# Kernel tuning notes

Measured on AMD Instinct MI355X. Metric: run time of the kernel, lower is better.

## Reference

```python
import jax, jax.numpy as jnp
import numpy as np

DIM = 1024
HEADS = 16
HEAD_DIM = DIM // HEADS
MLP_HIDDEN = int(DIM * 0.7)  # 716
EPS = 1e-5


def _ln(x, g, b):
    m = jnp.mean(x, axis=-1, keepdims=True)
    v = jnp.mean(jnp.square(x - m), axis=-1, keepdims=True)
    return (x - m) * jax.lax.rsqrt(v + EPS) * g + b


def setup_inputs() -> dict:
    key = jax.random.key(0)
    ks = jax.random.split(key, 8)
    B, N = 4, 1024
    x = jax.random.normal(ks[0], (B, N, DIM), dtype=jnp.float32)
    s = 0.02
    return {
        "x": x,
        "norm_g": jnp.ones((DIM,), jnp.float32),
        "norm_b": jnp.zeros((DIM,), jnp.float32),
        "W1": jax.random.normal(ks[1], (DIM, 3 * DIM + MLP_HIDDEN), jnp.float32) * s,
        "b1": jnp.zeros((3 * DIM + MLP_HIDDEN,), jnp.float32),
        "qn_g": jnp.ones((HEAD_DIM,), jnp.float32),
        "qn_b": jnp.zeros((HEAD_DIM,), jnp.float32),
        "kn_g": jnp.ones((HEAD_DIM,), jnp.float32),
        "kn_b": jnp.zeros((HEAD_DIM,), jnp.float32),
        "projW": jax.random.normal(ks[2], (DIM, DIM), jnp.float32) * s,
        "projb": jnp.zeros((DIM,), jnp.float32),
        "mlpW": jax.random.normal(ks[3], (MLP_HIDDEN, DIM), jnp.float32) * s,  # mlp_bias=False
        "W2": jax.random.normal(ks[4], (2 * DIM, DIM), jnp.float32) * s,
        "b2": jnp.zeros((DIM,), jnp.float32),
        "ls_g": jnp.full((DIM,), 1e-5, jnp.float32),
    }


def reference(x, norm_g, norm_b, W1, b1, qn_g, qn_b, kn_g, kn_b,
              projW, projb, mlpW, W2, b2, ls_g):
    B, N, C = x.shape
    norm_x = _ln(x, norm_g, norm_b)
    f1 = norm_x @ W1 + b1  # (B, N, 3*dim + mlp_hidden)
    qkv, mlp_hidden = f1[..., :3 * DIM], f1[..., 3 * DIM:]
    # (B, N, 3, H, hd) -> (3, B, H, N, hd)
    qkv = qkv.reshape(B, N, 3, HEADS, HEAD_DIM).transpose(2, 0, 3, 1, 4)
    q, k, v = qkv[0], qkv[1], qkv[2]
    q = _ln(q, qn_g, qn_b)
    k = _ln(k, kn_g, kn_b)
    attn = jnp.einsum('bhnd,bhmd->bhnm', q, k) * (HEAD_DIM ** -0.5)
    attn = jax.nn.softmax(attn, axis=-1)
    xo = jnp.einsum('bhnm,bhmd->bhnd', attn, v)
    xo = xo.transpose(0, 2, 1, 3).reshape(B, N, DIM)
    attn_out = xo @ projW + projb
    mlp_out = jax.nn.gelu(mlp_hidden, approximate=False) @ mlpW  # no bias
    combined = jnp.concatenate([attn_out, mlp_out], axis=-1)
    out = x + (combined @ W2 + b2) * ls_g
    return out
```

## Files before the change

### kernel.cpp

```cpp
#include <hip/hip_runtime.h>
#include <cstdint>
#include <cstddef>

typedef unsigned short u16;
typedef unsigned char u8;
typedef __attribute__((ext_vector_type(8))) u16 u16x8;
typedef __attribute__((ext_vector_type(8))) __bf16 bf16x8;
typedef __attribute__((ext_vector_type(4))) float f32x4;
typedef __attribute__((ext_vector_type(16))) float f32x16;
typedef __attribute__((ext_vector_type(4))) int i32x4;
typedef __attribute__((ext_vector_type(8))) int i32x8;
typedef __attribute__((ext_vector_type(2))) int i32x2;

__device__ __forceinline__ u16 f2bf(float f) {
  unsigned u = __builtin_bit_cast(unsigned, f);
  return (u16)((u + 0x7FFFu + ((u >> 16) & 1u)) >> 16);
}
__device__ __forceinline__ float bf2f(u16 h) {
  return __builtin_bit_cast(float, (unsigned)h << 16);
}
__device__ __forceinline__ u8 f2fp8(float f) {
  return (u8)(__builtin_amdgcn_cvt_pk_fp8_f32(f, 0.f, 0, false) & 0xFF);
}
__device__ __forceinline__ f32x4 mfma16(u16x8 a, u16x8 b, f32x4 c) {
  return __builtin_amdgcn_mfma_f32_16x16x32_bf16(
      __builtin_bit_cast(bf16x8, a), __builtin_bit_cast(bf16x8, b), c, 0, 0, 0);
}
__device__ __forceinline__ f32x16 mfma32(u16x8 a, u16x8 b, f32x16 c) {
  return __builtin_amdgcn_mfma_f32_32x32x16_bf16(
      __builtin_bit_cast(bf16x8, a), __builtin_bit_cast(bf16x8, b), c, 0, 0, 0);
}
__device__ __forceinline__ unsigned cvtpk_bf16(float lo, float hi) {
  unsigned r;
  asm("v_cvt_pk_bf16_f32 %0, %1, %2" : "=v"(r) : "v"(lo), "v"(hi));
  return r;
}
__device__ __forceinline__ void plswap(unsigned& a, unsigned& b) {
  i32x2 r = __builtin_amdgcn_permlane32_swap((int)a, (int)b, false, false);
  a = (unsigned)r[0];
  b = (unsigned)r[1];
}
__device__ __forceinline__ void load_lds16(const void* g, void* l) {
  __builtin_amdgcn_global_load_lds(
      (const __attribute__((address_space(1))) void*)g,
      (__attribute__((address_space(3))) void*)l, 16, 0, 0);
}

__global__ __launch_bounds__(256) void k_pre(
    const float* __restrict__ W1, const float* __restrict__ projW,
    const float* __restrict__ mlpW, const float* __restrict__ W2,
    u8* __restrict__ W1t, u8* __restrict__ pWt, u8* __restrict__ mWt,
    u8* __restrict__ W2t, const float* __restrict__ x,
    const float* __restrict__ g, const float* __restrict__ b,
    u8* __restrict__ nx8) {
  __shared__ float t[32][33];
  __shared__ float red[8];
  const int L = blockIdx.x;
  const int tid = threadIdx.x;
  if (L < 7680) {
    const float* src;
    u8* dst;
    int R, C, dR, dC, bx, by;
    if (L < 3840) {
      src = W1; dst = W1t; R = 1024; C = 3788; dR = 1024; dC = 3840;
      bx = L % 120; by = L / 120;
    } else if (L < 4864) {
      int tq = L - 3840;
      src = projW; dst = pWt; R = 1024; C = 1024; dR = 1024; dC = 1024;
      bx = tq & 31; by = tq >> 5;
    } else if (L < 5632) {
      int tq = L - 4864;
      src = mlpW; dst = mWt; R = 716; C = 1024; dR = 768; dC = 1024;
      bx = tq & 31; by = tq >> 5;
    } else {
      int tq = L - 5632;
      src = W2; dst = W2t; R = 2048; C = 1024; dR = 2048; dC = 1024;
      bx = tq & 31; by = tq >> 5;
    }
    const int n0 = bx * 32, k0 = by * 32;
    const int tx = tid & 31, ty = tid >> 5;
#pragma unroll
    for (int j = 0; j < 4; ++j) {
      int kk = k0 + ty + 8 * j, nn = n0 + tx;
      float v = (kk < R && nn < C) ? src[(size_t)kk * C + nn] : 0.f;
      t[ty + 8 * j][tx] = v;
    }
    __syncthreads();
#pragma unroll
    for (int j = 0; j < 4; ++j) {
      int nn = n0 + ty + 8 * j, kk = k0 + tx;
      if (nn < dC && kk < dR) dst[(size_t)nn * dR + kk] = f2fp8(t[tx][ty + 8 * j]);
    }
  } else {
    const int row = L - 7680;
    float4 v = ((const float4*)(x + (size_t)row * 1024))[tid];
    float s = v.x + v.y + v.z + v.w;
    float ss = v.x * v.x + v.y * v.y + v.z * v.z + v.w * v.w;
#pragma unroll
    for (int off = 1; off < 64; off <<= 1) {
      s += __shfl_xor(s, off);
      ss += __shfl_xor(ss, off);
    }
    const int wid = tid >> 6, lane = tid & 63;
    if (lane == 0) { red[wid] = s; red[4 + wid] = ss; }
    __syncthreads();
    s = red[0] + red[1] + red[2] + red[3];
    ss = red[4] + red[5] + red[6] + red[7];
    const float mean = s * (1.f / 1024.f);
    const float var = ss * (1.f / 1024.f) - mean * mean;
    const float rstd = rsqrtf(var + 1e-5f);
    float4 gv = ((const float4*)g)[tid];
    float4 bv = ((const float4*)b)[tid];
    float y0 = (v.x - mean) * rstd * gv.x + bv.x;
    float y1 = (v.y - mean) * rstd * gv.y + bv.y;
    float y2 = (v.z - mean) * rstd * gv.z + bv.z;
    float y3 = (v.w - mean) * rstd * gv.w + bv.w;
    int pk = __builtin_amdgcn_cvt_pk_fp8_f32(y0, y1, 0, false);
    pk = __builtin_amdgcn_cvt_pk_fp8_f32(y2, y3, pk, true);
    ((int*)(nx8 + (size_t)row * 1024))[tid] = pk;
  }
}

__device__ __forceinline__ void gemm_fp8_core(const u8* __restrict__ A,
                                              const u8* __restrict__ B, int K,
                                              u8* Alds, u8* Blds,
                                              f32x16 (&acc)[2][2], int tid) {
  const int lane = tid & 63, wave = tid >> 6;
  const int h = lane >> 5, r32 = lane & 31;
  const int wrow = (wave >> 1) * 64, wcol = (wave & 1) * 64;
  const int srow0 = tid >> 2, spos = tid & 3;
  const int nk = K >> 6;
#pragma unroll
  for (int p = 0; p < 2; ++p) {
    const int row = p * 64 + srow0;
    const int c = spos ^ ((row >> 1) & 3);
    const size_t go = (size_t)row * K + c * 16;
    load_lds16(A + go, Alds + (p * 256 + tid) * 16);
    load_lds16(B + go, Blds + (p * 256 + tid) * 16);
  }
  __syncthreads();
  for (int kt = 0; kt < nk; ++kt) {
    const int cur = kt & 1;
    const u8* Ac = Alds + cur * 8192;
    const u8* Bc = Blds + cur * 8192;
    if (kt + 1 < nk) {
      u8* An = Alds + (cur ^ 1) * 8192;
      u8* Bn = Blds + (cur ^ 1) * 8192;
#pragma unroll
      for (int p = 0; p < 2; ++p) {
        const int row = p * 64 + srow0;
        const int c = spos ^ ((row >> 1) & 3);
        const size_t go = (size_t)row * K + (size_t)(kt + 1) * 64 + c * 16;
        load_lds16(A + go, An + (p * 256 + tid) * 16);
        load_lds16(B + go, Bn + (p * 256 + tid) * 16);
      }
    }
    i32x8 af[2], bf[2];
#pragma unroll
    for (int t = 0; t < 2; ++t) {
      {
        const int row = wrow + t * 32 + r32;
        const int sw = (row >> 1) & 3;
        i32x4 lo = *(const i32x4*)(Ac + row * 64 + ((2 * h) ^ sw) * 16);
        i32x4 hi = *(const i32x4*)(Ac + row * 64 + ((2 * h + 1) ^ sw) * 16);
        i32x8 a;
        a[0] = lo[0]; a[1] = lo[1]; a[2] = lo[2]; a[3] = lo[3];
        a[4] = hi[0]; a[5] = hi[1]; a[6] = hi[2]; a[7] = hi[3];
        af[t] = a;
      }
      {
        const int row = wcol + t * 32 + r32;
        const int sw = (row >> 1) & 3;
        i32x4 lo = *(const i32x4*)(Bc + row * 64 + ((2 * h) ^ sw) * 16);
        i32x4 hi = *(const i32x4*)(Bc + row * 64 + ((2 * h + 1) ^ sw) * 16);
        i32x8 b8;
        b8[0] = lo[0]; b8[1] = lo[1]; b8[2] = lo[2]; b8[3] = lo[3];
        b8[4] = hi[0]; b8[5] = hi[1]; b8[6] = hi[2]; b8[7] = hi[3];
        bf[t] = b8;
      }
    }
#pragma unroll
    for (int i = 0; i < 2; ++i)
#pragma unroll
      for (int j = 0; j < 2; ++j)
        acc[i][j] = __builtin_amdgcn_mfma_scale_f32_32x32x64_f8f6f4(
            af[i], bf[j], acc[i][j], 0, 0, 0, 0x7F7F7F7F, 0, 0x7F7F7F7F);
    __syncthreads();
  }
}

__device__ __forceinline__ void gemm_fp8_core64(const u8* __restrict__ A,
                                                const u8* __restrict__ B, int K,
                                                u8* Alds, u8* Blds,
                                                f32x16 (&acc)[2], int tid) {
  const int lane = tid & 63, wave = tid >> 6;
  const int h = lane >> 5, r32 = lane & 31;
  const int wrow = (wave >> 1) * 32, wcol = (wave & 1) * 64;
  const int nk = K >> 6;
  const int ra = tid >> 2, posa = tid & 3;
  const int ca = posa ^ ((ra >> 1) & 3);
  load_lds16(A + (size_t)ra * K + ca * 16, Alds + tid * 16);
#pragma unroll
  for (int p = 0; p < 2; ++p) {
    const int s = tid + 256 * p;
    const int r = s >> 2, pos = s & 3;
    const int c = pos ^ ((r >> 1) & 3);
    load_lds16(B + (size_t)r * K + c * 16, Blds + s * 16);
  }
  __syncthreads();
  for (int kt = 0; kt < nk; ++kt) {
    const int cur = kt & 1;
    const u8* Ac = Alds + cur * 4096;
    const u8* Bc = Blds + cur * 8192;
    if (kt + 1 < nk) {
      u8* An = Alds + (cur ^ 1) * 4096;
      u8* Bn = Blds + (cur ^ 1) * 8192;
      const size_t k1 = (size_t)(kt + 1) * 64;
      load_lds16(A + (size_t)ra * K + k1 + ca * 16, An + tid * 16);
#pragma unroll
      for (int p = 0; p < 2; ++p) {
        const int s = tid + 256 * p;
        const int r = s >> 2, pos = s & 3;
        const int c = pos ^ ((r >> 1) & 3);
        load_lds16(B + (size_t)r * K + k1 + c * 16, Bn + s * 16);
      }
    }
    i32x8 af, bf[2];
    {
      const int row = wrow + r32;
      const int sw = (row >> 1) & 3;
      i32x4 lo = *(const i32x4*)(Ac + row * 64 + ((2 * h) ^ sw) * 16);
      i32x4 hi = *(const i32x4*)(Ac + row * 64 + ((2 * h + 1) ^ sw) * 16);
      af[0] = lo[0]; af[1] = lo[1]; af[2] = lo[2]; af[3] = lo[3];
      af[4] = hi[0]; af[5] = hi[1]; af[6] = hi[2]; af[7] = hi[3];
    }
#pragma unroll
    for (int t = 0; t < 2; ++t) {
      const int row = wcol + t * 32 + r32;
      const int sw = (row >> 1) & 3;
      i32x4 lo = *(const i32x4*)(Bc + row * 64 + ((2 * h) ^ sw) * 16);
      i32x4 hi = *(const i32x4*)(Bc + row * 64 + ((2 * h + 1) ^ sw) * 16);
      i32x8 b8;
      b8[0] = lo[0]; b8[1] = lo[1]; b8[2] = lo[2]; b8[3] = lo[3];
      b8[4] = hi[0]; b8[5] = hi[1]; b8[6] = hi[2]; b8[7] = hi[3];
      bf[t] = b8;
    }
#pragma unroll
    for (int j = 0; j < 2; ++j)
      acc[j] = __builtin_amdgcn_mfma_scale_f32_32x32x64_f8f6f4(
          af, bf[j], acc[j], 0, 0, 0, 0x7F7F7F7F, 0, 0x7F7F7F7F);
    __syncthreads();
  }
}

__global__ __launch_bounds__(256) void k_gemm1(const u8* __restrict__ nx8,
                                               const u8* __restrict__ W1t,
                                               u16* __restrict__ f1,
                                               const float* __restrict__ b1) {
  __shared__ __align__(16) u8 Alds[2 * 128 * 64];
  __shared__ __align__(16) u8 Blds[2 * 128 * 64];
  const int tid = threadIdx.x, bm = blockIdx.y, bn = blockIdx.x;
  f32x16 acc[2][2];
#pragma unroll
  for (int i = 0; i < 2; ++i)
#pragma unroll
    for (int j = 0; j < 2; ++j)
#pragma unroll
      for (int r = 0; r < 16; ++r) acc[i][j][r] = 0.f;
  gemm_fp8_core(nx8 + (size_t)bm * 128 * 1024, W1t + (size_t)bn * 128 * 1024, 1024,
                Alds, Blds, acc, tid);
  const int lane = tid & 63, wave = tid >> 6;
  const int h = lane >> 5, r32 = lane & 31;
  const int wrow = (wave >> 1) * 64, wcol = (wave & 1) * 64;
#pragma unroll
  for (int i = 0; i < 2; ++i)
#pragma unroll
    for (int j = 0; j < 2; ++j) {
      const int col = bn * 128 + wcol + j * 32 + r32;
      const float bs = (col < 3788) ? b1[col] : 0.f;
#pragma unroll
      for (int r = 0; r < 16; ++r) {
        const int row = bm * 128 + wrow + i * 32 + 4 * h + (r & 3) + 8 * (r >> 2);
        f1[(size_t)row * 3840 + col] = f2bf(acc[i][j][r] + bs);
      }
    }
}

__global__ __launch_bounds__(256) void k_gemm_pm(
    const u8* __restrict__ xo, const u8* __restrict__ pWt,
    const u8* __restrict__ gel, const u8* __restrict__ mWt,
    u8* __restrict__ comb, const float* __restrict__ projb) {
  __shared__ __align__(16) u8 Alds[2 * 64 * 64];
  __shared__ __align__(16) u8 Blds[2 * 128 * 64];
  const int tid = threadIdx.x, bm = blockIdx.y, bnq = blockIdx.x;
  const u8* A;
  const u8* B;
  int K, colbase;
  const float* bias;
  if (bnq < 8) {
    A = xo + (size_t)bm * 64 * 1024;
    B = pWt + (size_t)bnq * 128 * 1024;
    K = 1024; colbase = bnq * 128; bias = projb;
  } else {
    A = gel + (size_t)bm * 64 * 768;
    B = mWt + (size_t)(bnq - 8) * 128 * 768;
    K = 768; colbase = 1024 + (bnq - 8) * 128; bias = nullptr;
  }
  f32x16 acc[2];
#pragma unroll
  for (int j = 0; j < 2; ++j)
#pragma unroll
    for (int r = 0; r < 16; ++r) acc[j][r] = 0.f;
  gemm_fp8_core64(A, B, K, Alds, Blds, acc, tid);
  const int lane = tid & 63, wave = tid >> 6;
  const int h = lane >> 5, r32 = lane & 31;
  const int wrow = (wave >> 1) * 32, wcol = (wave & 1) * 64;
#pragma unroll
  for (int j = 0; j < 2; ++j) {
    const int col = colbase + wcol + j * 32 + r32;
    const float bs = (bias != nullptr) ? bias[col] : 0.f;
#pragma unroll
    for (int r = 0; r < 16; ++r) {
      const int row = bm * 64 + wrow + 4 * h + (r & 3) + 8 * (r >> 2);
      comb[(size_t)row * 2048 + col] = f2fp8(acc[j][r] + bs);
    }
  }
}

__global__ __launch_bounds__(256) void k_gemm_fin(const u8* __restrict__ comb,
                                                  const u8* __restrict__ W2t,
                                                  float* __restrict__ out,
                                                  const float* __restrict__ b2,
                                                  const float* __restrict__ x,
                                                  const float* __restrict__ lsg) {
  __shared__ __align__(16) u8 Alds[2 * 64 * 64];
  __shared__ __align__(16) u8 Blds[2 * 128 * 64];
  const int tid = threadIdx.x, bm = blockIdx.y, bn = blockIdx.x;
  f32x16 acc[2];
#pragma unroll
  for (int j = 0; j < 2; ++j)
#pragma unroll
    for (int r = 0; r < 16; ++r) acc[j][r] = 0.f;
  gemm_fp8_core64(comb + (size_t)bm * 64 * 2048, W2t + (size_t)bn * 128 * 2048, 2048,
                  Alds, Blds, acc, tid);
  const int lane = tid & 63, wave = tid >> 6;
  const int h = lane >> 5, r32 = lane & 31;
  const int wrow = (wave >> 1) * 32, wcol = (wave & 1) * 64;
#pragma unroll
  for (int j = 0; j < 2; ++j) {
    const int col = bn * 128 + wcol + j * 32 + r32;
    const float bs = b2[col], ls = lsg[col];
#pragma unroll
    for (int r = 0; r < 16; ++r) {
      const int row = bm * 64 + wrow + 4 * h + (r & 3) + 8 * (r >> 2);
      out[(size_t)row * 1024 + col] =
          x[(size_t)row * 1024 + col] + (acc[j][r] + bs) * ls;
    }
  }
}

__global__ __launch_bounds__(256) void k_mid(const u16* __restrict__ f1,
                                             const float* __restrict__ qg,
                                             const float* __restrict__ qbb,
                                             const float* __restrict__ kg,
                                             const float* __restrict__ kbb,
                                             u16* __restrict__ q,
                                             u16* __restrict__ k,
                                             u8* __restrict__ gel,
                                             u16* __restrict__ vtb) {
  __shared__ u16 tt[32][33];
  const int tid = threadIdx.x;
  const int L = blockIdx.x;
  if (L < 4096) {
    const int row = L;
    const int rem = tid >> 3;
    const int which = rem >> 4, h = rem & 15;
    const int e8 = (tid & 7) * 8;
    u16x8 xv = *(const u16x8*)(f1 + (size_t)row * 3840 + which * 1024 + h * 64 + e8);
    float xf[8];
    float s1 = 0.f, s2 = 0.f;
#pragma unroll
    for (int e = 0; e < 8; ++e) {
      xf[e] = bf2f(xv[e]);
      s1 += xf[e];
      s2 += xf[e] * xf[e];
    }
#pragma unroll
    for (int off = 1; off < 8; off <<= 1) {
      s1 += __shfl_xor(s1, off);
      s2 += __shfl_xor(s2, off);
    }
    const float mean = s1 * (1.f / 64.f);
    const float var = s2 * (1.f / 64.f) - mean * mean;
    const float rstd = rsqrtf(var + 1e-5f);
    const float* g = (which == 0) ? qg : kg;
    const float* bb = (which == 0) ? qbb : kbb;
    float4 g0 = ((const float4*)g)[e8 >> 2], g1 = ((const float4*)g)[(e8 >> 2) + 1];
    float4 b0 = ((const float4*)bb)[e8 >> 2], b1 = ((const float4*)bb)[(e8 >> 2) + 1];
    float gv[8] = {g0.x, g0.y, g0.z, g0.w, g1.x, g1.y, g1.z, g1.w};
    float bv[8] = {b0.x, b0.y, b0.z, b0.w, b1.x, b1.y, b1.z, b1.w};
    u16x8 o;
#pragma unroll
    for (int e = 0; e < 8; ++e) o[e] = f2bf((xf[e] - mean) * rstd * gv[e] + bv[e]);
    const int b = row >> 10, n = row & 1023;
    u16* dst = (which == 0) ? q : k;
    *(u16x8*)(dst + ((size_t)(b * 16 + h) * 1024 + n) * 64 + e8) = o;
  } else if (L < 5632) {
    const int id = (L - 4096) * 256 + tid;
    const int row = id / 96, c8 = id - row * 96;
    u16x8 xv = *(const u16x8*)(f1 + (size_t)row * 3840 + 3072 + c8 * 8);
    float rr[8];
#pragma unroll
    for (int e = 0; e < 8; ++e) {
      const int col = c8 * 8 + e;
      rr[e] = 0.f;
      if (col < 716) {
        float xx = bf2f(xv[e]);
        rr[e] = 0.5f * xx * (1.f + erff(xx * 0.70710678118654752f));
      }
    }
    int p0 = __builtin_amdgcn_cvt_pk_fp8_f32(rr[0], rr[1], 0, false);
    p0 = __builtin_amdgcn_cvt_pk_fp8_f32(rr[2], rr[3], p0, true);
    int p1 = __builtin_amdgcn_cvt_pk_fp8_f32(rr[4], rr[5], 0, false);
    p1 = __builtin_amdgcn_cvt_pk_fp8_f32(rr[6], rr[7], p1, true);
    uint2 pk;
    pk.x = (unsigned)p0;
    pk.y = (unsigned)p1;
    *(uint2*)(gel + (size_t)row * 768 + c8 * 8) = pk;
  } else {
    const int t = L - 5632;
    const int xq = t & 1, yq = (t >> 1) & 31, z = t >> 6;
    const int b = z >> 4, h = z & 15;
    const int d0 = xq * 32, n0 = yq * 32;
    const int tx = tid & 31, ty = tid >> 5;
#pragma unroll
    for (int j = 0; j < 4; ++j)
      tt[ty + 8 * j][tx] =
          f1[(size_t)(b * 1024 + n0 + ty + 8 * j) * 3840 + 2048 + h * 64 + d0 + tx];
    __syncthreads();
#pragma unroll
    for (int j = 0; j < 4; ++j)
      vtb[(size_t)z * 65536 + (size_t)(d0 + ty + 8 * j) * 1024 + n0 + tx] =
          tt[tx][ty + 8 * j];
  }
}

__global__ __launch_bounds__(128) void k_flash(const u16* __restrict__ q,
                                               const u16* __restrict__ k,
                                               const u16* __restrict__ vt,
                                               u8* __restrict__ xo) {
  __shared__ __align__(16) u16 Kl[2][64 * 64];
  __shared__ __align__(16) u16 Vl[2][64 * 64];
  const int tid = threadIdx.x, wave = tid >> 6, lane = tid & 63;
  const int l31 = lane & 31, h = lane >> 5;
  const int L = blockIdx.x;
  const int xcd = L & 7, i = L >> 3;
  const int bh = xcd * 8 + (i & 7), qt = i >> 3;
  const int qrow0 = qt * 64 + wave * 32;
  const u16* qb = q + ((size_t)bh * 1024 + qrow0) * 64;
  const u16* kb = k + (size_t)bh * 1024 * 64;
  const u16* vb = vt + (size_t)bh * 64 * 1024;

  u16x8 qf[4];
#pragma unroll
  for (int ds = 0; ds < 4; ++ds)
    qf[ds] = *(const u16x8*)(qb + (size_t)l31 * 64 + ds * 16 + h * 8);

  f32x16 O[2];
#pragma unroll
  for (int d2 = 0; d2 < 2; ++d2)
#pragma unroll
    for (int r = 0; r < 16; ++r) O[d2][r] = 0.f;
  float lacc = 0.f;

  int sr[4], sc[4];
#pragma unroll
  for (int p = 0; p < 4; ++p) {
    const int s = tid + 128 * p;
    sr[p] = s >> 3;
    sc[p] = (s & 7) ^ (sr[p] & 7);
  }

#pragma unroll
  for (int p = 0; p < 4; ++p) {
    const int s = tid + 128 * p;
    load_lds16(kb + (size_t)sr[p] * 64 + sc[p] * 8, (u16*)Kl[0] + s * 8);
    load_lds16(vb + (size_t)sr[p] * 1024 + sc[p] * 8, (u16*)Vl[0] + s * 8);
  }
  __syncthreads();

  for (int kv = 0; kv < 16; ++kv) {
    const int cur = kv & 1;
    if (kv < 15) {
      const size_t ko = (size_t)(kv + 1) * 64;
#pragma unroll
      for (int p = 0; p < 4; ++p) {
        const int s = tid + 128 * p;
        load_lds16(kb + (ko + sr[p]) * 64 + sc[p] * 8, (u16*)Kl[cur ^ 1] + s * 8);
        load_lds16(vb + (size_t)sr[p] * 1024 + ko + sc[p] * 8,
                   (u16*)Vl[cur ^ 1] + s * 8);
      }
    }
    const u16* Kc = (const u16*)Kl[cur];
    const u16* Vc = (const u16*)Vl[cur];

    f32x16 S[2];
#pragma unroll
    for (int t2 = 0; t2 < 2; ++t2)
#pragma unroll
      for (int r = 0; r < 16; ++r) S[t2][r] = 0.f;
    __builtin_amdgcn_s_setprio(1);
#pragma unroll
    for (int t2 = 0; t2 < 2; ++t2) {
      const int kr = t2 * 32 + l31;
      const int sw = kr & 7;
#pragma unroll
      for (int ds = 0; ds < 4; ++ds) {
        const int pos = (ds * 2 + h) ^ sw;
        u16x8 kf = *(const u16x8*)(Kc + kr * 64 + pos * 8);
        S[t2] = mfma32(kf, qf[ds], S[t2]);
      }
    }
    __builtin_amdgcn_s_setprio(0);

#pragma unroll
    for (int t2 = 0; t2 < 2; ++t2)
#pragma unroll
      for (int r = 0; r < 16; ++r) {
        float pv = __expf(S[t2][r] * 0.125f);
        S[t2][r] = pv;
        lacc += pv;
      }

    __builtin_amdgcn_s_setprio(1);
#pragma unroll
    for (int m = 0; m < 4; ++m) {
      const int t2 = m >> 1, ro = (m & 1) * 8;
      unsigned w0 = cvtpk_bf16(S[t2][ro + 0], S[t2][ro + 1]);
      unsigned w2 = cvtpk_bf16(S[t2][ro + 4], S[t2][ro + 5]);
      unsigned w1 = cvtpk_bf16(S[t2][ro + 2], S[t2][ro + 3]);
      unsigned w3 = cvtpk_bf16(S[t2][ro + 6], S[t2][ro + 7]);
      plswap(w0, w2);
      plswap(w1, w3);
      i32x4 aw;
      aw[0] = (int)w0; aw[1] = (int)w1; aw[2] = (int)w2; aw[3] = (int)w3;
      const u16x8 pa = __builtin_bit_cast(u16x8, aw);
#pragma unroll
      for (int d2 = 0; d2 < 2; ++d2) {
        const int vr = d2 * 32 + l31;
        const int pos = (m * 2 + h) ^ (vr & 7);
        u16x8 vf = *(const u16x8*)(Vc + vr * 64 + pos * 8);
        O[d2] = mfma32(pa, vf, O[d2]);
      }
    }
    __builtin_amdgcn_s_setprio(0);
    __syncthreads();
  }

  lacc += __shfl_xor(lacc, 32);
  const float inv = 1.f / lacc;
  const int b = bh >> 4, hh = bh & 15;
#pragma unroll
  for (int r = 0; r < 16; ++r) {
    const int qr = (r & 3) + 8 * (r >> 2) + 4 * h;
    const float invr = __shfl(inv, qr);
    u8* orow = xo + (size_t)(b * 1024 + qrow0 + qr) * 1024 + hh * 64;
    orow[l31] = f2fp8(O[0][r] * invr);
    orow[32 + l31] = f2fp8(O[1][r] * invr);
  }
}

extern "C" void kernel_launch(void* const* d_in, const int* in_sizes, int n_in,
                              void* d_out, int out_size, void* d_ws, size_t ws_size,
                              hipStream_t stream) {
  (void)in_sizes; (void)n_in; (void)out_size; (void)ws_size;
  const float* x      = (const float*)d_in[0];
  const float* norm_g = (const float*)d_in[1];
  const float* norm_b = (const float*)d_in[2];
  const float* W1     = (const float*)d_in[3];
  const float* b1     = (const float*)d_in[4];
  const float* qn_g   = (const float*)d_in[5];
  const float* qn_b   = (const float*)d_in[6];
  const float* kn_g   = (const float*)d_in[7];
  const float* kn_b   = (const float*)d_in[8];
  const float* projW  = (const float*)d_in[9];
  const float* projb  = (const float*)d_in[10];
  const float* mlpW   = (const float*)d_in[11];
  const float* W2     = (const float*)d_in[12];
  const float* b2     = (const float*)d_in[13];
  const float* ls_g   = (const float*)d_in[14];

  char* ws = (char*)d_ws;
  u8*  W1t8 = (u8*)(ws + 0);
  u8*  pWt8 = (u8*)(ws + 3932160);
  u8*  mWt8 = (u8*)(ws + 4980736);
  u8*  W2t8 = (u8*)(ws + 5767168);
  u8*  nx8  = (u8*)(ws + 7864320);
  u16* f1   = (u16*)(ws + 12058624);
  u16* qbuf = (u16*)(ws + 43515904);
  u16* kbuf = (u16*)(ws + 51904512);
  u16* vtb  = (u16*)(ws + 60293120);
  u8*  gel8 = (u8*)(ws + 68681728);

  k_pre<<<11776, 256, 0, stream>>>(W1, projW, mlpW, W2, W1t8, pWt8, mWt8, W2t8,
                                   x, norm_g, norm_b, nx8);
  k_gemm1<<<dim3(30, 32), 256, 0, stream>>>(nx8, W1t8, f1, b1);
  k_mid<<<9728, 256, 0, stream>>>(f1, qn_g, qn_b, kn_g, kn_b, qbuf, kbuf, gel8,
                                  vtb);
  k_flash<<<1024, 128, 0, stream>>>(qbuf, kbuf, vtb, nx8);
  k_gemm_pm<<<dim3(16, 64), 256, 0, stream>>>(nx8, pWt8, gel8, mWt8, (u8*)f1, projb);
  k_gemm_fin<<<dim3(8, 64), 256, 0, stream>>>((u8*)f1, W2t8, (float*)d_out, b2, x,
                                              ls_g);
}
```

Measured before the change: 228.8 us.

## Triple-buffer FP8 GEMM LDS staging with vmcnt-based waits instead of syncthreads

Turns the double-buffered global-to-LDS pipeline in both FP8 GEMM cores into a three-stage ring, issuing loads two K-tiles ahead. The full __syncthreads at the end of each iteration is replaced by a partial s_waitcnt vmcnt plus s_barrier, so the next tile's loads can stay in flight while the current MFMAs run. The aim is to hide global memory latency better. In exchange, LDS use per block grows by half, which may lower occupancy, and the hand-counted vmcnt values must match exactly how many loads each stage issues.

Result: faster. 223.4 us (-2.4%).

```diff
diff --git a/kernel.cpp b/kernel.cpp
--- a/kernel.cpp
+++ b/kernel.cpp
@@ -130,31 +130,24 @@
   const int wrow = (wave >> 1) * 64, wcol = (wave & 1) * 64;
   const int srow0 = tid >> 2, spos = tid & 3;
   const int nk = K >> 6;
-#pragma unroll
-  for (int p = 0; p < 2; ++p) {
-    const int row = p * 64 + srow0;
-    const int c = spos ^ ((row >> 1) & 3);
-    const size_t go = (size_t)row * K + c * 16;
-    load_lds16(A + go, Alds + (p * 256 + tid) * 16);
-    load_lds16(B + go, Blds + (p * 256 + tid) * 16);
-  }
-  __syncthreads();
+  auto STAGE = [&](int t, int bb) {
+#pragma unroll
+    for (int p = 0; p < 2; ++p) {
+      const int row = p * 64 + srow0;
+      const int c = spos ^ ((row >> 1) & 3);
+      const size_t go = (size_t)row * K + (size_t)t * 64 + c * 16;
+      load_lds16(A + go, Alds + bb * 8192 + (p * 256 + tid) * 16);
+      load_lds16(B + go, Blds + bb * 8192 + (p * 256 + tid) * 16);
+    }
+  };
+  STAGE(0, 0);
+  STAGE(1, 1);
+  asm volatile("s_waitcnt vmcnt(4)" ::: "memory");
+  __builtin_amdgcn_s_barrier();
+  int cur = 0;
   for (int kt = 0; kt < nk; ++kt) {
-    const int cur = kt & 1;
     const u8* Ac = Alds + cur * 8192;
     const u8* Bc = Blds + cur * 8192;
-    if (kt + 1 < nk) {
-      u8* An = Alds + (cur ^ 1) * 8192;
-      u8* Bn = Blds + (cur ^ 1) * 8192;
-#pragma unroll
-      for (int p = 0; p < 2; ++p) {
-        const int row = p * 64 + srow0;
-        const int c = spos ^ ((row >> 1) & 3);
-        const size_t go = (size_t)row * K + (size_t)(kt + 1) * 64 + c * 16;
-        load_lds16(A + go, An + (p * 256 + tid) * 16);
-        load_lds16(B + go, Bn + (p * 256 + tid) * 16);
-      }
-    }
     i32x8 af[2], bf[2];
 #pragma unroll
     for (int t = 0; t < 2; ++t) {
@@ -179,13 +172,21 @@
         bf[t] = b8;
       }
     }
+    if (kt + 2 < nk) STAGE(kt + 2, cur == 0 ? 2 : cur - 1);
 #pragma unroll
     for (int i = 0; i < 2; ++i)
 #pragma unroll
       for (int j = 0; j < 2; ++j)
         acc[i][j] = __builtin_amdgcn_mfma_scale_f32_32x32x64_f8f6f4(
             af[i], bf[j], acc[i][j], 0, 0, 0, 0x7F7F7F7F, 0, 0x7F7F7F7F);
-    __syncthreads();
+    if (kt + 1 < nk) {
+      if (kt + 2 < nk)
+        asm volatile("s_waitcnt vmcnt(4)" ::: "memory");
+      else
+        asm volatile("s_waitcnt vmcnt(0)" ::: "memory");
+      __builtin_amdgcn_s_barrier();
+    }
+    cur = (cur == 2) ? 0 : cur + 1;
   }
 }
 
@@ -199,32 +200,25 @@
   const int nk = K >> 6;
   const int ra = tid >> 2, posa = tid & 3;
   const int ca = posa ^ ((ra >> 1) & 3);
-  load_lds16(A + (size_t)ra * K + ca * 16, Alds + tid * 16);
-#pragma unroll
-  for (int p = 0; p < 2; ++p) {
-    const int s = tid + 256 * p;
-    const int r = s >> 2, pos = s & 3;
-    const int c = pos ^ ((r >> 1) & 3);
-    load_lds16(B + (size_t)r * K + c * 16, Blds + s * 16);
-  }
-  __syncthreads();
+  auto STAGE = [&](int t, int bb) {
+    const size_t k0 = (size_t)t * 64;
+    load_lds16(A + (size_t)ra * K + k0 + ca * 16, Alds + bb * 4096 + tid * 16);
+#pragma unroll
+    for (int p = 0; p < 2; ++p) {
+      const int s = tid + 256 * p;
+      const int r = s >> 2, pos = s & 3;
+      const int c = pos ^ ((r >> 1) & 3);
+      load_lds16(B + (size_t)r * K + k0 + c * 16, Blds + bb * 8192 + s * 16);
+    }
+  };
+  STAGE(0, 0);
+  STAGE(1, 1);
+  asm volatile("s_waitcnt vmcnt(3)" ::: "memory");
+  __builtin_amdgcn_s_barrier();
+  int cur = 0;
   for (int kt = 0; kt < nk; ++kt) {
-    const int cur = kt & 1;
     const u8* Ac = Alds + cur * 4096;
     const u8* Bc = Blds + cur * 8192;
-    if (kt + 1 < nk) {
-      u8* An = Alds + (cur ^ 1) * 4096;
-      u8* Bn = Blds + (cur ^ 1) * 8192;
-      const size_t k1 = (size_t)(kt + 1) * 64;
-      load_lds16(A + (size_t)ra * K + k1 + ca * 16, An + tid * 16);
-#pragma unroll
-      for (int p = 0; p < 2; ++p) {
-        const int s = tid + 256 * p;
-        const int r = s >> 2, pos = s & 3;
-        const int c = pos ^ ((r >> 1) & 3);
-        load_lds16(B + (size_t)r * K + k1 + c * 16, Bn + s * 16);
-      }
-    }
     i32x8 af, bf[2];
     {
       const int row = wrow + r32;
@@ -245,11 +239,19 @@
       b8[4] = hi[0]; b8[5] = hi[1]; b8[6] = hi[2]; b8[7] = hi[3];
       bf[t] = b8;
     }
+    if (kt + 2 < nk) STAGE(kt + 2, cur == 0 ? 2 : cur - 1);
 #pragma unroll
     for (int j = 0; j < 2; ++j)
       acc[j] = __builtin_amdgcn_mfma_scale_f32_32x32x64_f8f6f4(
           af, bf[j], acc[j], 0, 0, 0, 0x7F7F7F7F, 0, 0x7F7F7F7F);
-    __syncthreads();
+    if (kt + 1 < nk) {
+      if (kt + 2 < nk)
+        asm volatile("s_waitcnt vmcnt(3)" ::: "memory");
+      else
+        asm volatile("s_waitcnt vmcnt(0)" ::: "memory");
+      __builtin_amdgcn_s_barrier();
+    }
+    cur = (cur == 2) ? 0 : cur + 1;
   }
 }
 
@@ -257,8 +259,8 @@
                                                const u8* __restrict__ W1t,
                                                u16* __restrict__ f1,
                                                const float* __restrict__ b1) {
-  __shared__ __align__(16) u8 Alds[2 * 128 * 64];
-  __shared__ __align__(16) u8 Blds[2 * 128 * 64];
+  __shared__ __align__(16) u8 Alds[3 * 128 * 64];
+  __shared__ __align__(16) u8 Blds[3 * 128 * 64];
   const int tid = threadIdx.x, bm = blockIdx.y, bn = blockIdx.x;
   f32x16 acc[2][2];
 #pragma unroll
@@ -290,8 +292,8 @@
     const u8* __restrict__ xo, const u8* __restrict__ pWt,
     const u8* __restrict__ gel, const u8* __restrict__ mWt,
     u8* __restrict__ comb, const float* __restrict__ projb) {
-  __shared__ __align__(16) u8 Alds[2 * 64 * 64];
-  __shared__ __align__(16) u8 Blds[2 * 128 * 64];
+  __shared__ __align__(16) u8 Alds[3 * 64 * 64];
+  __shared__ __align__(16) u8 Blds[3 * 128 * 64];
   const int tid = threadIdx.x, bm = blockIdx.y, bnq = blockIdx.x;
   const u8* A;
   const u8* B;
@@ -333,8 +335,8 @@
                                                   const float* __restrict__ b2,
                                                   const float* __restrict__ x,
                                                   const float* __restrict__ lsg) {
-  __shared__ __align__(16) u8 Alds[2 * 64 * 64];
-  __shared__ __align__(16) u8 Blds[2 * 128 * 64];
+  __shared__ __align__(16) u8 Alds[3 * 64 * 64];
+  __shared__ __align__(16) u8 Blds[3 * 128 * 64];
   const int tid = threadIdx.x, bm = blockIdx.y, bn = blockIdx.x;
   f32x16 acc[2];
 #pragma unroll
```
